# Kernel optimization log

Hardware: AMD Instinct MI355X
Metric: run time of the kernel (lower is better)

The kernel has to match this reference:

```python
import jax, jax.numpy as jnp
import numpy as np

N_EMBD = 1024
N_HEAD = 16
DIM_HEAD = N_EMBD // N_HEAD
SCALE = DIM_HEAD ** (-0.5)  # source divides by this (i.e. multiplies scores by sqrt(dim_head))


def setup_inputs() -> dict:
    key = jax.random.key(0)
    k1, k2, k3, k4, k5 = jax.random.split(key, 5)
    B, Tq, Tkv = 2, 2048, 2048
    x_q = jax.random.normal(k1, (B, Tq, N_EMBD), dtype=jnp.float32)
    x_kv = jax.random.normal(k2, (B, Tkv, N_EMBD), dtype=jnp.float32)
    s = 0.02
    W_q = jax.random.normal(k3, (N_EMBD, N_EMBD), dtype=jnp.float32) * s
    W_kv = jax.random.normal(k4, (N_EMBD, 2 * N_EMBD), dtype=jnp.float32) * s
    W_proj = jax.random.normal(k5, (N_EMBD, N_EMBD), dtype=jnp.float32) * s
    return {"x_q": x_q, "x_kv": x_kv, "W_q": W_q, "W_kv": W_kv, "W_proj": W_proj}


def reference(x_q, x_kv, W_q, W_kv, W_proj):
    B, Tq, C = x_q.shape
    Tkv = x_kv.shape[1]
    q = x_q @ W_q                      # [B, Tq, C]
    kv = x_kv @ W_kv                   # [B, Tkv, 2C]
    k, v = jnp.split(kv, 2, axis=2)
    # [B, H, T, Dh]
    q = q.reshape(B, Tq, N_HEAD, DIM_HEAD).transpose(0, 2, 1, 3)
    k = k.reshape(B, Tkv, N_HEAD, DIM_HEAD).transpose(0, 2, 1, 3)
    v = v.reshape(B, Tkv, N_HEAD, DIM_HEAD).transpose(0, 2, 1, 3)
    # Faithful to source: scores = q@k^T / scale  (== * sqrt(dim_head))
    attn = jnp.einsum('bhqd,bhkd->bhqk', q, k) / SCALE
    attn = jax.nn.softmax(attn, axis=-1)
    y = jnp.einsum('bhqk,bhkd->bhqd', attn, v)
    y = y.transpose(0, 2, 1, 3).reshape(B, Tq, C)
    return y @ W_proj
```

## Files before the change

### kernel.cpp

```cpp
#include <hip/hip_runtime.h>
#include <cstddef>

typedef _Float16 f16;
typedef _Float16 f16x8 __attribute__((ext_vector_type(8)));
typedef _Float16 f16x4 __attribute__((ext_vector_type(4)));
typedef _Float16 f16x2 __attribute__((ext_vector_type(2)));
typedef float f32x4 __attribute__((ext_vector_type(4)));
typedef float f32x16 __attribute__((ext_vector_type(16)));
typedef unsigned int u32;

__device__ inline float exp2_fast(float x) {
  float r;
  asm("v_exp_f32 %0, %1" : "=v"(r) : "v"(x));
  return r;
}

__device__ inline int pk2(float x, float y) {
  return __builtin_bit_cast(int, __builtin_amdgcn_cvt_pkrtz(x, y));
}

__device__ inline f16x2 pk2h(float x, float y) {
  return __builtin_bit_cast(f16x2, __builtin_amdgcn_cvt_pkrtz(x, y));
}

__device__ inline void permlane32_swap(int& a, int& b) {
  asm volatile("v_permlane32_swap_b32 %0, %1" : "+v"(a), "+v"(b));
}

__device__ __forceinline__ void gload16(const f16* g, f16* l) {
  __builtin_amdgcn_global_load_lds(
      (const __attribute__((address_space(1))) void*)g,
      (__attribute__((address_space(3))) void*)l, 16, 0, 0);
}

__global__ __launch_bounds__(256) void prep(
    const float* __restrict__ xq, const float* __restrict__ xkv,
    f16* __restrict__ oq, f16* __restrict__ okv,
    const float* __restrict__ Wq, const float* __restrict__ Wkv,
    const float* __restrict__ Wp, f16* __restrict__ Wqt,
    f16* __restrict__ Wkvt, f16* __restrict__ Wpt) {
  __shared__ float t[32][33];
  int bid = blockIdx.x;
  if (bid < 8192) {
    const float* in = (bid < 4096) ? xq : xkv;
    f16* out = (bid < 4096) ? oq : okv;
    int i = ((bid & 4095) * 256 + threadIdx.x) * 4;
    float4 v = *(const float4*)&in[i];
    f16x4 h;
    h[0] = (f16)v.x; h[1] = (f16)v.y; h[2] = (f16)v.z; h[3] = (f16)v.w;
    *(f16x4*)&out[i] = h;
  } else {
    int zz = bid - 8192;
    int bx = zz & 31, by = (zz >> 5) & 31, z = zz >> 10;
    const float* in;
    f16* out;
    int N = 1024, extra = 0;
    if (z == 0) { in = Wq; out = Wqt; }
    else if (z == 3) { in = Wp; out = Wpt; }
    else { in = Wkv; out = Wkvt; N = 2048; extra = (z - 1) * 1024; }
    int tx = threadIdx.x % 32, ty = threadIdx.x / 32;
    int n0 = bx * 32 + extra, k0 = by * 32;
#pragma unroll
    for (int i = 0; i < 32; i += 8)
      t[ty + i][tx] = in[(size_t)(k0 + ty + i) * N + n0 + tx];
    __syncthreads();
#pragma unroll
    for (int i = 0; i < 32; i += 8)
      out[(size_t)(n0 + ty + i) * 1024 + k0 + tx] = (f16)t[tx][ty + i];
  }
}

template <int BN, typename CT>
__device__ __forceinline__ void gemm_body(
    const f16* __restrict__ A, const f16* __restrict__ Bt, CT* __restrict__ C,
    int bid, int M, int N, int K, float scale, f16* As, f16* Bs) {
  constexpr int NT = BN / 32;
  constexpr int ASZ = 128 * 64;
  constexpr int BSZ = BN * 64;
  const int nb = N / BN;
  const int nwg = (M / 128) * nb;
  const int sbid = (bid & 7) * (nwg >> 3) + (bid >> 3);
  const int m0 = (sbid / nb) * 128;
  const int n0 = (sbid % nb) * BN;
  const int tid = threadIdx.x;
  const int w = tid >> 6, lane = tid & 63;
  const int l16 = lane & 15, quad = lane >> 4;
  const int wrow = (w >> 1) * 64, wcol = (w & 1) * (BN / 2);
  const int lrow = lane >> 3;
  const int lcs = (((lane & 7) ^ (lane >> 3)) & 7) * 8;

  f32x4 acc[4][NT] = {};

#define STAGE_TILE(bp, kk)                                                   \
  {                                                                          \
    _Pragma("unroll") for (int i = 0; i < 4; i++) {                          \
      const int r = w * 32 + i * 8;                                          \
      gload16(&A[(size_t)(m0 + r + lrow) * K + (kk) + lcs],                  \
              &As[(bp) * ASZ + r * 64]);                                     \
    }                                                                        \
    _Pragma("unroll") for (int i = 0; i < NT; i++) {                         \
      const int r = w * (BN / 4) + i * 8;                                    \
      gload16(&Bt[(size_t)(n0 + r + lrow) * K + (kk) + lcs],                 \
              &Bs[(bp) * BSZ + r * 64]);                                     \
    }                                                                        \
  }

#define VMCNT_TILE()                                                         \
  {                                                                          \
    if constexpr (NT == 4) {                                                 \
      asm volatile("s_waitcnt vmcnt(8)" ::: "memory");                       \
    } else {                                                                 \
      asm volatile("s_waitcnt vmcnt(6)" ::: "memory");                       \
    }                                                                        \
    __builtin_amdgcn_sched_barrier(0);                                       \
  }

  STAGE_TILE(0, 0);
  STAGE_TILE(1, 64);
  VMCNT_TILE();
  __builtin_amdgcn_s_barrier();

  int buf = 0;
  for (int k0 = 0; k0 < K; k0 += 64) {
    const f16* Asb = &As[buf * ASZ];
    const f16* Bsb = &Bs[buf * BSZ];

    f16x8 bf[NT][2];
#pragma unroll
    for (int nt = 0; nt < NT; nt++) {
      const int row = wcol + nt * 16 + l16;
#pragma unroll
      for (int s = 0; s < 2; s++)
        bf[nt][s] = *(const f16x8*)&Bsb[row * 64 + (((s * 4 + quad) ^ (row & 7)) << 3)];
    }
#pragma unroll
    for (int mt = 0; mt < 4; mt++) {
      const int row = wrow + mt * 16 + l16;
      f16x8 af0 = *(const f16x8*)&Asb[row * 64 + ((quad ^ (row & 7)) << 3)];
      f16x8 af1 = *(const f16x8*)&Asb[row * 64 + (((4 + quad) ^ (row & 7)) << 3)];
#pragma unroll
      for (int nt = 0; nt < NT; nt++) {
        acc[mt][nt] = __builtin_amdgcn_mfma_f32_16x16x32_f16(af0, bf[nt][0], acc[mt][nt], 0, 0, 0);
        acc[mt][nt] = __builtin_amdgcn_mfma_f32_16x16x32_f16(af1, bf[nt][1], acc[mt][nt], 0, 0, 0);
      }
    }

    __builtin_amdgcn_s_barrier();
    if (k0 + 128 < K) {
      STAGE_TILE(buf, k0 + 128);
      VMCNT_TILE();
    } else {
      asm volatile("s_waitcnt vmcnt(0)" ::: "memory");
      __builtin_amdgcn_sched_barrier(0);
    }
    __builtin_amdgcn_s_barrier();
    buf ^= 1;
  }
#undef STAGE_TILE
#undef VMCNT_TILE

#pragma unroll
  for (int mt = 0; mt < 4; mt++)
#pragma unroll
    for (int nt = 0; nt < NT; nt++)
#pragma unroll
      for (int r = 0; r < 4; r++) {
        int row = m0 + wrow + mt * 16 + quad * 4 + r;
        int col = n0 + wcol + nt * 16 + l16;
        C[(size_t)row * N + col] = (CT)(acc[mt][nt][r] * scale);
      }
}

__global__ __launch_bounds__(256, 2) void qkv_gemm(
    const f16* __restrict__ Xq, const f16* __restrict__ Wqt, f16* __restrict__ Qh,
    const f16* __restrict__ Xkv, const f16* __restrict__ Wkvt, f16* __restrict__ KVh,
    float sc_q) {
  __shared__ f16 As[2 * 128 * 64];
  __shared__ f16 Bs[2 * 128 * 64];
  if (blockIdx.x < 256)
    gemm_body<128, f16>(Xq, Wqt, Qh, blockIdx.x, 4096, 1024, 1024, sc_q, As, Bs);
  else
    gemm_body<128, f16>(Xkv, Wkvt, KVh, blockIdx.x - 256, 4096, 2048, 1024, 1.0f, As, Bs);
}

template <int BN, typename CT>
__global__ __launch_bounds__(256, 3) void gemm_lds(
    const f16* __restrict__ A, const f16* __restrict__ Bt, CT* __restrict__ C,
    int M, int N, int K, float scale) {
  __shared__ f16 As[2 * 128 * 64];
  __shared__ f16 Bs[2 * BN * 64];
  gemm_body<BN, CT>(A, Bt, C, blockIdx.x, M, N, K, scale, As, Bs);
}

__global__ __launch_bounds__(512, 4) void attn_kernel(
    const f16* __restrict__ Qh, const f16* __restrict__ KVh, f16* __restrict__ Yh) {
  __shared__ f16 smem[18432];

  const int bid = blockIdx.x;
  const int hb = bid & 31;
  const int qt = bid >> 5;
  const int h = hb >> 1, b = hb & 1;
  const int tid = threadIdx.x;
  const int w = tid >> 6, lane = tid & 63;
  const int l31 = lane & 31, e = lane >> 5;
  const int qw = w & 3, half = w >> 2;
  const int tl = tid & 255;

  f16* Ks = smem + half * (2 * 64 * 72);
  f16* Vt = Ks + 64 * 72;

  const size_t qrow0 = (size_t)b * 2048 + (size_t)qt * 128;
  const size_t kvrow0 = (size_t)b * 2048 + (size_t)half * 1024;

  f16x8 qf[4];
#pragma unroll
  for (int ks = 0; ks < 4; ks++)
    qf[ks] = *(const f16x8*)&Qh[(qrow0 + qw * 32 + l31) * 1024 + h * 64 + ks * 16 + e * 8];

  float m_run = -1e30f, l_run = 0.0f;
  f32x16 o_acc[2] = {};

  const int ksr = tl >> 2, ksc = (tl & 3) << 4;
  const int vkv0 = (tl >> 3) * 2;
  const int vd0 = (tl & 7) * 8;
  const int vcol = ((((vkv0 >> 3) ^ (tl & 7)) << 3) | (vkv0 & 7));

  f16x8 kr0, kr1, vr0, vr1;
  {
    const f16* kb = &KVh[(kvrow0 + ksr) * 2048 + h * 64 + ksc];
    kr0 = *(const f16x8*)kb;
    kr1 = *(const f16x8*)(kb + 8);
    const f16* vb = &KVh[(kvrow0 + vkv0) * 2048 + 1024 + h * 64 + vd0];
    vr0 = *(const f16x8*)vb;
    vr1 = *(const f16x8*)(vb + 2048);
  }

  for (int t = 0; t < 16; t++) {
    *(f16x8*)&Ks[ksr * 72 + ksc] = kr0;
    *(f16x8*)&Ks[ksr * 72 + ksc + 8] = kr1;
#pragma unroll
    for (int j = 0; j < 8; j++) {
      f16x2 p; p[0] = vr0[j]; p[1] = vr1[j];
      *(f16x2*)&Vt[(vd0 + j) * 72 + vcol] = p;
    }
    __syncthreads();

    if (t + 1 < 16) {
      const f16* kb = &KVh[(kvrow0 + (t + 1) * 64 + ksr) * 2048 + h * 64 + ksc];
      kr0 = *(const f16x8*)kb;
      kr1 = *(const f16x8*)(kb + 8);
      const f16* vb = &KVh[(kvrow0 + (t + 1) * 64 + vkv0) * 2048 + 1024 + h * 64 + vd0];
      vr0 = *(const f16x8*)vb;
      vr1 = *(const f16x8*)(vb + 2048);
    }

    f32x16 sacc[2] = {};
#pragma unroll
    for (int kvt = 0; kvt < 2; kvt++)
#pragma unroll
      for (int ks = 0; ks < 4; ks++) {
        f16x8 a = *(const f16x8*)&Ks[(kvt * 32 + l31) * 72 + ks * 16 + e * 8];
        sacc[kvt] = __builtin_amdgcn_mfma_f32_32x32x16_f16(a, qf[ks], sacc[kvt], 0, 0, 0);
      }

    float mxa[4];
#pragma unroll
    for (int j = 0; j < 4; j++) {
      float a = fmaxf(fmaxf(sacc[0][j], sacc[0][j + 4]),
                      fmaxf(sacc[0][j + 8], sacc[0][j + 12]));
      float bb = fmaxf(fmaxf(sacc[1][j], sacc[1][j + 4]),
                       fmaxf(sacc[1][j + 8], sacc[1][j + 12]));
      mxa[j] = fmaxf(a, bb);
    }
    float mx = fmaxf(fmaxf(mxa[0], mxa[1]), fmaxf(mxa[2], mxa[3]));
    mx = fmaxf(mx, __shfl_xor(mx, 32, 64));

    if (!__all(mx <= m_run + 8.0f)) {
      float mnew = fmaxf(m_run, mx);
      float alpha = exp2_fast(m_run - mnew);
      m_run = mnew;
      l_run *= alpha;
#pragma unroll
      for (int r = 0; r < 16; r++) { o_acc[0][r] *= alpha; o_acc[1][r] *= alpha; }
    }

    float ss0 = 0.0f, ss1 = 0.0f, ss2 = 0.0f, ss3 = 0.0f;
#pragma unroll
    for (int kvt = 0; kvt < 2; kvt++)
#pragma unroll
      for (int r = 0; r < 16; r += 4) {
        float p0 = exp2_fast(sacc[kvt][r + 0] - m_run);
        float p1 = exp2_fast(sacc[kvt][r + 1] - m_run);
        float p2 = exp2_fast(sacc[kvt][r + 2] - m_run);
        float p3 = exp2_fast(sacc[kvt][r + 3] - m_run);
        sacc[kvt][r + 0] = p0; sacc[kvt][r + 1] = p1;
        sacc[kvt][r + 2] = p2; sacc[kvt][r + 3] = p3;
        ss0 += p0; ss1 += p1; ss2 += p2; ss3 += p3;
      }
    float ssum = (ss0 + ss1) + (ss2 + ss3);
    ssum += __shfl_xor(ssum, 32, 64);
    l_run += ssum;

    f16x8 pf[4];
#pragma unroll
    for (int kvt = 0; kvt < 2; kvt++)
#pragma unroll
      for (int hf = 0; hf < 2; hf++) {
        const int h8 = hf * 8;
        int a0 = pk2(sacc[kvt][h8 + 0], sacc[kvt][h8 + 1]);
        int b0 = pk2(sacc[kvt][h8 + 4], sacc[kvt][h8 + 5]);
        int a1 = pk2(sacc[kvt][h8 + 2], sacc[kvt][h8 + 3]);
        int b1 = pk2(sacc[kvt][h8 + 6], sacc[kvt][h8 + 7]);
        permlane32_swap(a0, b0);
        permlane32_swap(a1, b1);
        union { int i[4]; f16x8 v; } u;
        u.i[0] = a0; u.i[1] = a1; u.i[2] = b0; u.i[3] = b1;
        pf[kvt * 2 + hf] = u.v;
      }

#pragma unroll
    for (int dt = 0; dt < 2; dt++) {
      const int d = dt * 32 + l31;
      const int dx = d >> 3;
#pragma unroll
      for (int ks = 0; ks < 4; ks++) {
        f16x8 va = *(const f16x8*)&Vt[d * 72 + (((ks * 2 + e) ^ dx) << 3)];
        o_acc[dt] = __builtin_amdgcn_mfma_f32_32x32x16_f16(va, pf[ks], o_acc[dt], 0, 0, 0);
      }
    }
    __syncthreads();
  }

  float* Om = (float*)smem;
  float* ML = (float*)smem + 4 * 32 * 68;
  if (half == 1) {
#pragma unroll
    for (int dt = 0; dt < 2; dt++)
#pragma unroll
      for (int r2 = 0; r2 < 4; r2++) {
        f32x4 vv;
        vv[0] = o_acc[dt][r2 * 4 + 0];
        vv[1] = o_acc[dt][r2 * 4 + 1];
        vv[2] = o_acc[dt][r2 * 4 + 2];
        vv[3] = o_acc[dt][r2 * 4 + 3];
        *(f32x4*)&Om[(qw * 32 + l31) * 68 + dt * 32 + r2 * 8 + e * 4] = vv;
      }
    ML[qw * 64 + l31] = m_run;
    ML[qw * 64 + 32 + l31] = l_run;
  }
  __syncthreads();
  float linv = 0.0f;
  if (half == 0) {
    float m1 = ML[qw * 64 + l31], l1 = ML[qw * 64 + 32 + l31];
    float mm = fmaxf(m_run, m1);
    float a0 = exp2_fast(m_run - mm), a1 = exp2_fast(m1 - mm);
    linv = 1.0f / (l_run * a0 + l1 * a1);
#pragma unroll
    for (int dt = 0; dt < 2; dt++)
#pragma unroll
      for (int r2 = 0; r2 < 4; r2++) {
        f32x4 o1 = *(const f32x4*)&Om[(qw * 32 + l31) * 68 + dt * 32 + r2 * 8 + e * 4];
#pragma unroll
        for (int j = 0; j < 4; j++)
          o_acc[dt][r2 * 4 + j] = o_acc[dt][r2 * 4 + j] * a0 + o1[j] * a1;
      }
  }
  __syncthreads();

  if (half == 0) {
    f16* Of = smem + qw * 32 * 72;
#pragma unroll
    for (int dt = 0; dt < 2; dt++)
#pragma unroll
      for (int r2 = 0; r2 < 4; r2++) {
        f16x2 h0 = pk2h(o_acc[dt][r2 * 4 + 0] * linv, o_acc[dt][r2 * 4 + 1] * linv);
        f16x2 h1 = pk2h(o_acc[dt][r2 * 4 + 2] * linv, o_acc[dt][r2 * 4 + 3] * linv);
        f16x4 hh; hh[0] = h0[0]; hh[1] = h0[1]; hh[2] = h1[0]; hh[3] = h1[1];
        *(f16x4*)&Of[l31 * 72 + dt * 32 + r2 * 8 + e * 4] = hh;
      }
    const int qq = lane >> 1, dh = (lane & 1) * 32;
#pragma unroll
    for (int j = 0; j < 4; j++) {
      f16x8 v = *(const f16x8*)&Of[qq * 72 + dh + j * 8];
      *(f16x8*)&Yh[(qrow0 + qw * 32 + qq) * 1024 + h * 64 + dh + j * 8] = v;
    }
  }
}

extern "C" void kernel_launch(void* const* d_in, const int* in_sizes, int n_in,
                              void* d_out, int out_size, void* d_ws, size_t ws_size,
                              hipStream_t stream) {
  const float* x_q  = (const float*)d_in[0];
  const float* x_kv = (const float*)d_in[1];
  const float* W_q  = (const float*)d_in[2];
  const float* W_kv = (const float*)d_in[3];
  const float* W_p  = (const float*)d_in[4];
  float* out = (float*)d_out;

  f16* Wq_t  = (f16*)d_ws;
  f16* Wkv_t = Wq_t  + (size_t)1024 * 1024;
  f16* Wp_t  = Wkv_t + (size_t)2048 * 1024;
  f16* Qh    = Wp_t  + (size_t)1024 * 1024;
  f16* KVh   = Qh    + (size_t)4096 * 1024;
  f16* Yh    = KVh   + (size_t)4096 * 2048;
  f16* Xq_h  = Yh;
  f16* Xkv_h = Yh    + (size_t)4096 * 1024;

  prep<<<12288, 256, 0, stream>>>(x_q, x_kv, Xq_h, Xkv_h,
                                  W_q, W_kv, W_p, Wq_t, Wkv_t, Wp_t);

  const float SC = 11.5415603f;
  qkv_gemm<<<768, 256, 0, stream>>>(Xq_h, Wq_t, Qh, Xkv_h, Wkv_t, KVh, SC);

  attn_kernel<<<512, 512, 0, stream>>>(Qh, KVh, Yh);

  gemm_lds<64, float><<<512, 256, 0, stream>>>(Yh, Wp_t, out, 4096, 1024, 1024, 1.0f);
}
```

Baseline: 204.5 us.

## Double-buffer K/V tiles in LDS and raise MFMA priority in attention

The attention loop now keeps two LDS buffers for K and transposed V. While the current tile is being used for QK^T, the next tile is written from registers into the other buffer and the tile after that is prefetched from global memory. This leaves one barrier per iteration instead of two. MFMA sections are wrapped in s_setprio to favour matrix issue across waves. LDS use doubles to 72KB per block, which may reduce how many blocks fit per CU, and prefetched registers are held longer.

Measured after the change: 212.1 us. 1.04x slower.

```diff
diff --git a/kernel.cpp b/kernel.cpp
--- a/kernel.cpp
+++ b/kernel.cpp
@@ -194,7 +194,7 @@
 
 __global__ __launch_bounds__(512, 4) void attn_kernel(
     const f16* __restrict__ Qh, const f16* __restrict__ KVh, f16* __restrict__ Yh) {
-  __shared__ f16 smem[18432];
+  __shared__ f16 smem[36864];
 
   const int bid = blockIdx.x;
   const int hb = bid & 31;
@@ -206,8 +206,7 @@
   const int qw = w & 3, half = w >> 2;
   const int tl = tid & 255;
 
-  f16* Ks = smem + half * (2 * 64 * 72);
-  f16* Vt = Ks + 64 * 72;
+  f16* KsBase = smem + half * 18432;
 
   const size_t qrow0 = (size_t)b * 2048 + (size_t)qt * 128;
   const size_t kvrow0 = (size_t)b * 2048 + (size_t)half * 1024;
@@ -235,33 +234,59 @@
     vr1 = *(const f16x8*)(vb + 2048);
   }
 
-  for (int t = 0; t < 16; t++) {
-    *(f16x8*)&Ks[ksr * 72 + ksc] = kr0;
-    *(f16x8*)&Ks[ksr * 72 + ksc + 8] = kr1;
+  {
+    f16* K0 = KsBase;
+    f16* V0 = KsBase + 4608;
+    *(f16x8*)&K0[ksr * 72 + ksc] = kr0;
+    *(f16x8*)&K0[ksr * 72 + ksc + 8] = kr1;
 #pragma unroll
     for (int j = 0; j < 8; j++) {
       f16x2 p; p[0] = vr0[j]; p[1] = vr1[j];
-      *(f16x2*)&Vt[(vd0 + j) * 72 + vcol] = p;
-    }
-    __syncthreads();
+      *(f16x2*)&V0[(vd0 + j) * 72 + vcol] = p;
+    }
+    const f16* kb = &KVh[(kvrow0 + 64 + ksr) * 2048 + h * 64 + ksc];
+    kr0 = *(const f16x8*)kb;
+    kr1 = *(const f16x8*)(kb + 8);
+    const f16* vb = &KVh[(kvrow0 + 64 + vkv0) * 2048 + 1024 + h * 64 + vd0];
+    vr0 = *(const f16x8*)vb;
+    vr1 = *(const f16x8*)(vb + 2048);
+  }
+  __syncthreads();
+
+  for (int t = 0; t < 16; t++) {
+    f16* Kc = KsBase + (t & 1) * 9216;
+    f16* Vc = Kc + 4608;
+    f16* Kn = KsBase + ((t + 1) & 1) * 9216;
+    f16* Vn = Kn + 4608;
+
+    f32x16 sacc[2] = {};
+    __builtin_amdgcn_s_setprio(1);
+#pragma unroll
+    for (int kvt = 0; kvt < 2; kvt++)
+#pragma unroll
+      for (int ks = 0; ks < 4; ks++) {
+        f16x8 a = *(const f16x8*)&Kc[(kvt * 32 + l31) * 72 + ks * 16 + e * 8];
+        sacc[kvt] = __builtin_amdgcn_mfma_f32_32x32x16_f16(a, qf[ks], sacc[kvt], 0, 0, 0);
+      }
+    __builtin_amdgcn_s_setprio(0);
 
     if (t + 1 < 16) {
-      const f16* kb = &KVh[(kvrow0 + (t + 1) * 64 + ksr) * 2048 + h * 64 + ksc];
+      *(f16x8*)&Kn[ksr * 72 + ksc] = kr0;
+      *(f16x8*)&Kn[ksr * 72 + ksc + 8] = kr1;
+#pragma unroll
+      for (int j = 0; j < 8; j++) {
+        f16x2 p; p[0] = vr0[j]; p[1] = vr1[j];
+        *(f16x2*)&Vn[(vd0 + j) * 72 + vcol] = p;
+      }
+    }
+    if (t + 2 < 16) {
+      const f16* kb = &KVh[(kvrow0 + (t + 2) * 64 + ksr) * 2048 + h * 64 + ksc];
       kr0 = *(const f16x8*)kb;
       kr1 = *(const f16x8*)(kb + 8);
-      const f16* vb = &KVh[(kvrow0 + (t + 1) * 64 + vkv0) * 2048 + 1024 + h * 64 + vd0];
+      const f16* vb = &KVh[(kvrow0 + (t + 2) * 64 + vkv0) * 2048 + 1024 + h * 64 + vd0];
       vr0 = *(const f16x8*)vb;
       vr1 = *(const f16x8*)(vb + 2048);
     }
-
-    f32x16 sacc[2] = {};
-#pragma unroll
-    for (int kvt = 0; kvt < 2; kvt++)
-#pragma unroll
-      for (int ks = 0; ks < 4; ks++) {
-        f16x8 a = *(const f16x8*)&Ks[(kvt * 32 + l31) * 72 + ks * 16 + e * 8];
-        sacc[kvt] = __builtin_amdgcn_mfma_f32_32x32x16_f16(a, qf[ks], sacc[kvt], 0, 0, 0);
-      }
 
     float mxa[4];
 #pragma unroll
@@ -318,16 +343,19 @@
         pf[kvt * 2 + hf] = u.v;
       }
 
+    __builtin_amdgcn_s_setprio(1);
 #pragma unroll
     for (int dt = 0; dt < 2; dt++) {
       const int d = dt * 32 + l31;
       const int dx = d >> 3;
 #pragma unroll
       for (int ks = 0; ks < 4; ks++) {
-        f16x8 va = *(const f16x8*)&Vt[d * 72 + (((ks * 2 + e) ^ dx) << 3)];
+        f16x8 va = *(const f16x8*)&Vc[d * 72 + (((ks * 2 + e) ^ dx) << 3)];
         o_acc[dt] = __builtin_amdgcn_mfma_f32_32x32x16_f16(va, pf[ks], o_acc[dt], 0, 0, 0);
       }
     }
+    __builtin_amdgcn_s_setprio(0);
+
     __syncthreads();
   }
 
```
